# Kernel tuning notes

Hardware: AMD Instinct MI355X
Metric: run time of the kernel (lower is better)

Reference implementation:

```python
import jax, jax.numpy as jnp
import numpy as np

_J6 = jnp.array([[0, 0, 0, 0, 0, 1], [0, 0, 0, 0, -1, 0], [0, 0, 0, 1, 0, 0],
                 [0, 0, 1, 0, 0, 0], [0, -1, 0, 0, 0, 0], [1, 0, 0, 0, 0, 0]], dtype=jnp.float32)
_PAIRS4 = [(0, 1), (0, 2), (0, 3), (1, 2), (1, 3), (2, 3)]


def exterior(p1, p2):
    # p1, p2: (B,T,H,4) -> (B,T,H,6) normalized Pluecker line coordinates
    parts = [p1[..., i] * p2[..., j] - p1[..., j] * p2[..., i] for i, j in _PAIRS4]
    L = jnp.stack(parts, axis=-1)
    n = jnp.sqrt(jnp.sum(L * L, axis=-1, keepdims=True))
    return L / jnp.maximum(n, 1e-12)


def setup_inputs() -> dict:
    D, H = 1024, 16
    B, T = 2, 2048
    key = jax.random.key(0)
    ks = jax.random.split(key, 16)
    s = 0.02
    return {
        'x': jax.random.normal(ks[0], (B, T, D), dtype=jnp.float32),
        'qkv_w': jax.random.normal(ks[1], (D, 3 * D), dtype=jnp.float32) * s,
        'qkv_b': jnp.zeros((3 * D,), dtype=jnp.float32),
        'w1_write': jax.random.normal(ks[2], (D, 4 * H), dtype=jnp.float32) * s,
        'w2_write': jax.random.normal(ks[3], (D, 4 * H), dtype=jnp.float32) * s,
        'w1_read': jax.random.normal(ks[4], (D, 4 * H), dtype=jnp.float32) * s,
        'w2_read': jax.random.normal(ks[5], (D, 4 * H), dtype=jnp.float32) * s,
        'geo_w': jax.random.normal(ks[6], (D, D), dtype=jnp.float32) * s,
        'geo_b': jnp.zeros((D,), dtype=jnp.float32),
        'gate_w': jax.random.normal(ks[7], (D, H), dtype=jnp.float32) * s,
        'gate_b': jnp.zeros((H,), dtype=jnp.float32),
        'inc_scale': jnp.ones((H,), dtype=jnp.float32),
        'out_w': jax.random.normal(ks[8], (D, D), dtype=jnp.float32) * s,
        'out_b': jnp.zeros((D,), dtype=jnp.float32),
    }


def reference(x, qkv_w, qkv_b, w1_write, w2_write, w1_read, w2_read,
              geo_w, geo_b, gate_w, gate_b, inc_scale, out_w, out_b):
    B, T, D = x.shape
    H = inc_scale.shape[0]
    dh = D // H
    scale = dh ** -0.5

    qkv = (x @ qkv_w + qkv_b).reshape(B, T, 3, H, dh)
    qkv = jnp.transpose(qkv, (2, 0, 3, 1, 4))  # (3,B,H,T,dh)
    q, k, v = qkv[0], qkv[1], qkv[2]

    std_logits = jnp.einsum('bhqd,bhkd->bhqk', q, k) * scale

    x_prev = jnp.concatenate([jnp.zeros((B, 1, D), dtype=x.dtype), x[:, :-1]], axis=1)
    w1 = (x_prev @ w1_write).reshape(B, T, H, 4)
    w2 = (x @ w2_write).reshape(B, T, H, 4)
    write_lines = exterior(w1, w2)  # (B,T,H,6)
    r1 = (x @ w1_read).reshape(B, T, H, 4)
    r2 = (x @ w2_read).reshape(B, T, H, 4)
    read_lines = exterior(r1, r2)  # (B,T,H,6)

    J_write = jnp.einsum('bthi,ij->bthj', write_lines, _J6)  # (B,T,H,6)
    geo_logits = jnp.einsum('bqhi,bkhi->bhqk', read_lines, J_write)
    geo_logits = geo_logits * inc_scale.reshape(1, H, 1, 1)

    mask = jnp.triu(jnp.ones((T, T), dtype=bool), k=1)  # True above diagonal
    neg = jnp.float32(-jnp.inf)

    std_attn = jax.nn.softmax(jnp.where(mask, neg, std_logits), axis=-1)
    std_out = jnp.einsum('bhqk,bhkd->bqhd', std_attn, v).reshape(B, T, D)

    geo_attn = jax.nn.softmax(jnp.where(mask, neg, geo_logits), axis=-1)
    geo_v = (x @ geo_w + geo_b).reshape(B, T, H, dh)
    geo_out = jnp.einsum('bhqk,bkhd->bqhd', geo_attn, geo_v).reshape(B, T, D)

    gate = jax.nn.sigmoid(x @ gate_w + gate_b)  # (B,T,H)
    gate = jnp.mean(gate, axis=-1, keepdims=True)  # (B,T,1)

    combined = (1.0 - gate) * std_out + gate * geo_out
    return combined @ out_w + out_b
```

## Files before the change

kernel.cpp:

```cpp
#include <hip/hip_runtime.h>
#include <hip/hip_bf16.h>

#define Bc 2
#define Tc 2048
#define Dc 1024
#define Hc 16
#define Mc (Bc*Tc)
#define QB 64
#define KB 32
#define NALL 4480

typedef __attribute__((ext_vector_type(8))) short bf16x8;
typedef __attribute__((ext_vector_type(4))) short bf16x4;
typedef __attribute__((ext_vector_type(4))) float fx4;

__device__ __forceinline__ short f2bf(float f) {
  __hip_bfloat16 h = __float2bfloat16(f);
  return *reinterpret_cast<short*>(&h);
}
__device__ __forceinline__ float bf2f(short s) {
  unsigned int u = ((unsigned int)(unsigned short)s) << 16;
  float f;
  __builtin_memcpy(&f, &u, 4);
  return f;
}
__device__ __forceinline__ short p2bf(float f) {
  unsigned int u;
  __builtin_memcpy(&u, &f, 4);
  return (short)((u + 0x8000u) >> 16);
}

#define MFMA(a, b, c) __builtin_amdgcn_mfma_f32_16x16x32_bf16((a), (b), (c), 0, 0, 0)

#define GLD16(G, L) __builtin_amdgcn_global_load_lds( \
    (const __attribute__((address_space(1))) unsigned int*)(G), \
    (__attribute__((address_space(3))) unsigned int*)(L), 16, 0, 0)

__global__ __launch_bounds__(256) void f2b_k(const float* __restrict__ in,
                                             short* __restrict__ out) {
  const int i = blockIdx.x * 256 + threadIdx.x;
  const float4 v = ((const float4*)in)[i];
  bf16x4 o;
  o[0] = f2bf(v.x); o[1] = f2bf(v.y); o[2] = f2bf(v.z); o[3] = f2bf(v.w);
  ((bf16x4*)out)[i] = o;
}

__global__ void biasall_k(const float* __restrict__ qkv_b,
                          const float* __restrict__ geob,
                          const float* __restrict__ gateb,
                          float* __restrict__ ball) {
  const int n = blockIdx.x * 256 + threadIdx.x;
  if (n >= NALL) return;
  float v = 0.f;
  if (n < 1024)      v = qkv_b[n] * 0.125f;
  else if (n < 3072) v = qkv_b[n];
  else if (n < 4096) v = geob[n - 3072];
  else if (n >= 4352 && n < 4368) v = gateb[n - 4352];
  ball[n] = v;
}

__global__ __launch_bounds__(256) void tconv_all_k(
    const float* __restrict__ qkv_w, const float* __restrict__ geow,
    const float* __restrict__ w1w, const float* __restrict__ w2w,
    const float* __restrict__ w1r, const float* __restrict__ w2r,
    const float* __restrict__ gatew, short* __restrict__ wtall)
{
  __shared__ float tile[32][33];
  const int n0 = blockIdx.x * 32, k0 = blockIdx.y * 32;
  const int tx = threadIdx.x & 31, ty = threadIdx.x >> 5;
  const int n = n0 + tx;
  const float* src = nullptr; int ln = 0, sN = 0;
  if (n < 3072)      { src = qkv_w; ln = n;        sN = 3072; }
  else if (n < 4096) { src = geow;  ln = n - 3072; sN = 1024; }
  else if (n < 4160) { src = w1w;   ln = n - 4096; sN = 64; }
  else if (n < 4224) { src = w2w;   ln = n - 4160; sN = 64; }
  else if (n < 4288) { src = w1r;   ln = n - 4224; sN = 64; }
  else if (n < 4352) { src = w2r;   ln = n - 4288; sN = 64; }
  else if (n < 4368) { src = gatew; ln = n - 4352; sN = 16; }
  #pragma unroll
  for (int i = 0; i < 4; i++)
    tile[ty * 4 + i][tx] = src ? src[(size_t)(k0 + ty * 4 + i) * sN + ln] : 0.f;
  __syncthreads();
  #pragma unroll
  for (int i = 0; i < 4; i++) {
    const int nn = n0 + ty * 4 + i;
    const float s = (nn < 1024) ? 0.125f : 1.f;
    wtall[(size_t)nn * 1024 + k0 + tx] = f2bf(tile[tx][ty * 4 + i] * s);
  }
}

__global__ __launch_bounds__(256) void tconv_k(const float* __restrict__ W,
                                               short* __restrict__ Wt,
                                               int K, int N) {
  __shared__ float tile[32][33];
  const int k0 = blockIdx.y * 32, n0 = blockIdx.x * 32;
  const int tx = threadIdx.x & 31, ty = threadIdx.x >> 5;
  #pragma unroll
  for (int i = 0; i < 4; i++)
    tile[ty * 4 + i][tx] = W[(size_t)(k0 + ty * 4 + i) * N + n0 + tx];
  __syncthreads();
  #pragma unroll
  for (int i = 0; i < 4; i++)
    Wt[(size_t)(n0 + ty * 4 + i) * K + k0 + tx] = f2bf(tile[tx][ty * 4 + i]);
}

template<bool BF16_OUT>
__global__ __launch_bounds__(256) void gemm_mfma_k(
    const short* __restrict__ A, const short* __restrict__ Bt,
    const float* __restrict__ bias, void* __restrict__ Cv,
    int M, int N, int K)
{
  __shared__ short As[128][32];
  __shared__ short Bs[128][32];
  const int m0 = blockIdx.y * 128, n0 = blockIdx.x * 128;
  const int tid = threadIdx.x;
  const int wave = tid >> 6, lane = tid & 63;
  const int l15 = lane & 15, lg = lane >> 4;
  const int wm = wave >> 1, wn = wave & 1;
  const int srow = lane >> 2;
  const int schk = (lane & 3) * 8;

  const size_t aBase = (size_t)(m0 + wave * 16 + srow) * K + schk;
  const size_t bBase = (size_t)(n0 + wave * 16 + srow) * K + schk;

  fx4 acc[4][4] = {};

  for (int k0 = 0; k0 < K; k0 += 32) {
    __syncthreads();
    GLD16(&A[aBase + k0],              &As[wave * 16][0]);
    GLD16(&A[aBase + (size_t)64 * K + k0], &As[64 + wave * 16][0]);
    GLD16(&Bt[bBase + k0],             &Bs[wave * 16][0]);
    GLD16(&Bt[bBase + (size_t)64 * K + k0], &Bs[64 + wave * 16][0]);
    __syncthreads();
    bf16x8 af[4], bf[4];
    #pragma unroll
    for (int i = 0; i < 4; i++) {
      af[i] = *(const bf16x8*)&As[wm * 64 + i * 16 + l15][8 * lg];
      bf[i] = *(const bf16x8*)&Bs[wn * 64 + i * 16 + l15][8 * lg];
    }
    #pragma unroll
    for (int i = 0; i < 4; i++)
      #pragma unroll
      for (int j = 0; j < 4; j++)
        acc[i][j] = MFMA(af[i], bf[j], acc[i][j]);
  }

  #pragma unroll
  for (int i = 0; i < 4; i++)
    #pragma unroll
    for (int j = 0; j < 4; j++) {
      const int n = n0 + wn * 64 + j * 16 + l15;
      const float bv = bias ? bias[n] : 0.f;
      #pragma unroll
      for (int rg = 0; rg < 4; rg++) {
        const int m = m0 + wm * 64 + i * 16 + lg * 4 + rg;
        const float v = acc[i][j][rg] + bv;
        if constexpr (BF16_OUT)
          ((short*)Cv)[(size_t)m * N + n] = f2bf(v);
        else
          ((float*)Cv)[(size_t)m * N + n] = v;
      }
    }
}

template<bool BF16_OUT>
__global__ __launch_bounds__(256) void gemm_mfma64_k(
    const short* __restrict__ A, const short* __restrict__ Bt,
    const float* __restrict__ bias, void* __restrict__ Cv,
    int M, int N, int K)
{
  __shared__ short As[64][32];
  __shared__ short Bs[128][32];
  const int m0 = blockIdx.y * 64, n0 = blockIdx.x * 128;
  const int tid = threadIdx.x;
  const int wave = tid >> 6, lane = tid & 63;
  const int l15 = lane & 15, lg = lane >> 4;
  const int srow = lane >> 2;
  const int schk = (lane & 3) * 8;

  const size_t aBase = (size_t)(m0 + wave * 16 + srow) * K + schk;
  const size_t bBase = (size_t)(n0 + wave * 16 + srow) * K + schk;

  fx4 acc[4][2] = {};

  for (int k0 = 0; k0 < K; k0 += 32) {
    __syncthreads();
    GLD16(&A[aBase + k0],                   &As[wave * 16][0]);
    GLD16(&Bt[bBase + k0],                  &Bs[wave * 16][0]);
    GLD16(&Bt[bBase + (size_t)64 * K + k0], &Bs[64 + wave * 16][0]);
    __syncthreads();
    bf16x8 af[4], bf[2];
    #pragma unroll
    for (int i = 0; i < 4; i++)
      af[i] = *(const bf16x8*)&As[i * 16 + l15][8 * lg];
    #pragma unroll
    for (int j = 0; j < 2; j++)
      bf[j] = *(const bf16x8*)&Bs[wave * 32 + j * 16 + l15][8 * lg];
    #pragma unroll
    for (int i = 0; i < 4; i++)
      #pragma unroll
      for (int j = 0; j < 2; j++)
        acc[i][j] = MFMA(af[i], bf[j], acc[i][j]);
  }

  #pragma unroll
  for (int i = 0; i < 4; i++)
    #pragma unroll
    for (int j = 0; j < 2; j++) {
      const int n = n0 + wave * 32 + j * 16 + l15;
      const float bv = bias ? bias[n] : 0.f;
      #pragma unroll
      for (int rg = 0; rg < 4; rg++) {
        const int m = m0 + i * 16 + lg * 4 + rg;
        const float v = acc[i][j][rg] + bv;
        if constexpr (BF16_OUT)
          ((short*)Cv)[(size_t)m * N + n] = f2bf(v);
        else
          ((float*)Cv)[(size_t)m * N + n] = v;
      }
    }
}

__device__ __forceinline__ void exterior6(const float a[4], const float c[4], float L[6]) {
  L[0] = a[0]*c[1] - a[1]*c[0];
  L[1] = a[0]*c[2] - a[2]*c[0];
  L[2] = a[0]*c[3] - a[3]*c[0];
  L[3] = a[1]*c[2] - a[2]*c[1];
  L[4] = a[1]*c[3] - a[3]*c[1];
  L[5] = a[2]*c[3] - a[3]*c[2];
}

__device__ __forceinline__ void load4bf(const short* p, float o[4]) {
  const bf16x4 v = *(const bf16x4*)p;
  o[0] = bf2f(v[0]); o[1] = bf2f(v[1]); o[2] = bf2f(v[2]); o[3] = bf2f(v[3]);
}

__global__ void lines_k(const short* __restrict__ allb,
                        const float* __restrict__ incs,
                        short* __restrict__ JWb, short* __restrict__ RLb,
                        float* __restrict__ gatev)
{
  const int idx = blockIdx.x * 256 + threadIdx.x;
  if (idx >= Bc * Tc * Hc) return;
  const int h = idx & 15;
  const int t = (idx >> 4) & (Tc - 1);
  const int b = idx >> 15;
  const size_t row = (size_t)b * Tc + t;
  const size_t lrow = ((size_t)(b * Hc + h) * Tc + t) * 8;

  float a[4] = {0.f, 0.f, 0.f, 0.f};
  float c[4];
  load4bf(&allb[row * NALL + 4160 + h * 4], c);
  if (t > 0) load4bf(&allb[(row - 1) * NALL + 4096 + h * 4], a);

  float L[6];
  exterior6(a, c, L);
  float n = sqrtf(L[0]*L[0] + L[1]*L[1] + L[2]*L[2] + L[3]*L[3] + L[4]*L[4] + L[5]*L[5]);
  float inv = 1.f / fmaxf(n, 1e-12f);
  const float s = incs[h];
  bf16x8 jw;
  jw[0] = f2bf( L[5] * inv * s);
  jw[1] = f2bf(-L[4] * inv * s);
  jw[2] = f2bf( L[3] * inv * s);
  jw[3] = f2bf( L[2] * inv * s);
  jw[4] = f2bf(-L[1] * inv * s);
  jw[5] = f2bf( L[0] * inv * s);
  jw[6] = 0; jw[7] = 0;
  *(bf16x8*)&JWb[lrow] = jw;

  load4bf(&allb[row * NALL + 4224 + h * 4], a);
  load4bf(&allb[row * NALL + 4288 + h * 4], c);
  exterior6(a, c, L);
  n = sqrtf(L[0]*L[0] + L[1]*L[1] + L[2]*L[2] + L[3]*L[3] + L[4]*L[4] + L[5]*L[5]);
  inv = 1.f / fmaxf(n, 1e-12f);
  bf16x8 rl;
  #pragma unroll
  for (int i = 0; i < 6; i++) rl[i] = f2bf(L[i] * inv);
  rl[6] = 0; rl[7] = 0;
  *(bf16x8*)&RLb[lrow] = rl;

  if (h == 0) {
    float ssum = 0.f;
    #pragma unroll
    for (int hh = 0; hh < 16; hh++) {
      const float v = bf2f(allb[row * NALL + 4352 + hh]);
      ssum += 1.f / (1.f + __expf(-v));
    }
    gatev[row] = ssum * (1.f / 16.f);
  }
}

#define LOADK(K0, a0, a1, b0, b1) { \
  const size_t rb0 = (size_t)(b * Tc + (K0) + l15) * NALL + 1024 + h * 64; \
  const size_t rb1 = rb0 + (size_t)16 * NALL; \
  a0 = *(const bf16x8*)&allb[rb0 + lg * 8]; \
  a1 = *(const bf16x8*)&allb[rb0 + 32 + lg * 8]; \
  b0 = *(const bf16x8*)&allb[rb1 + lg * 8]; \
  b1 = *(const bf16x8*)&allb[rb1 + 32 + lg * 8]; }

#define LOADJW(K0, j0, j1) { \
  j0 = z8; j1 = z8; \
  if (lg == 0) { \
    j0 = *(const bf16x8*)&JWb[(size_t)(bh * Tc + (K0) + l15) * 8]; \
    j1 = *(const bf16x8*)&JWb[(size_t)(bh * Tc + (K0) + 16 + l15) * 8]; \
  } }

#define LOADVG(K0, vr, gr) { \
  vr = *(const bf16x8*)&allb[(size_t)(b * Tc + (K0) + kk) * NALL + 2048 + h * 64 + dg]; \
  gr = *(const bf16x8*)&allb[(size_t)(b * Tc + (K0) + kk) * NALL + 3072 + h * 64 + dg]; }

#define STAGEVG(CUR, vr, gr) { \
  _Pragma("unroll") for (int j = 0; j < 8; j++) { \
    const int d = dg + j; \
    const int col = ((kc2 ^ ((d >> 3) & 3)) << 3) | kl2; \
    Vt[CUR][d][col] = vr[j]; Gt[CUR][d][col] = gr[j]; \
  } }

#define COMPUTE(K0, CUR, ka0, ka1, kb0, kb1, jw0, jw1) \
  if ((K0) <= qhi) { \
    fx4 z = {0.f, 0.f, 0.f, 0.f}; \
    fx4 sS0, sS1, sG0, sG1; \
    __builtin_amdgcn_s_setprio(1); \
    sS0 = MFMA(qf0, ka0, z); sS0 = MFMA(qf1, ka1, sS0); \
    sS1 = MFMA(qf0, kb0, z); sS1 = MFMA(qf1, kb1, sS1); \
    sG0 = MFMA(rlf, jw0, z); sG1 = MFMA(rlf, jw1, z); \
    __builtin_amdgcn_s_setprio(0); \
    if ((K0) + KB - 1 > q0 + wave * 16) { \
      const int kg0 = (K0) + l15, kg1 = (K0) + 16 + l15; \
      _Pragma("unroll") for (int r = 0; r < 4; r++) { \
        const int qg = q0 + wave * 16 + lg * 4 + r; \
        if (kg0 > qg) { sS0[r] = -1e30f; sG0[r] = -1e30f; } \
        if (kg1 > qg) { sS1[r] = -1e30f; sG1[r] = -1e30f; } \
      } } \
    _Pragma("unroll") for (int r = 0; r < 4; r++) { \
      const int ql = lg * 4 + r; \
      const float p0 = __expf(sS0[r]); const float p1 = __expf(sS1[r]); \
      lpS[r] += p0 + p1; \
      Ps[wave][ql][l15] = p2bf(p0); Ps[wave][ql][16 + l15] = p2bf(p1); \
      const float g0 = __expf(sG0[r]); const float g1 = __expf(sG1[r]); \
      lpG[r] += g0 + g1; \
      Pg[wave][ql][l15] = p2bf(g0); Pg[wave][ql][16 + l15] = p2bf(g1); \
    } \
    const bf16x8 pa  = *(const bf16x8*)&Ps[wave][l15][8 * lg]; \
    const bf16x8 pga = *(const bf16x8*)&Pg[wave][l15][8 * lg]; \
    __builtin_amdgcn_s_setprio(1); \
    _Pragma("unroll") for (int dt = 0; dt < 4; dt++) { \
      const int dV = dt * 16 + l15; \
      const int swz = 8 * (lg ^ ((dV >> 3) & 3)); \
      accS[dt] = MFMA(pa,  *(const bf16x8*)&Vt[CUR][dV][swz], accS[dt]); \
      accG[dt] = MFMA(pga, *(const bf16x8*)&Gt[CUR][dV][swz], accG[dt]); \
    } \
    __builtin_amdgcn_s_setprio(0); \
  }

__global__ __launch_bounds__(256) void attn3_k(
    const short* __restrict__ allb,
    const short* __restrict__ RLb,
    const short* __restrict__ JWb,
    const float* __restrict__ gate,
    short* __restrict__ combb)
{
  const int orig = blockIdx.x;
  const int xcd  = orig & 7;
  const int idx  = orig >> 3;
  const int pairIdx = idx & 15;
  const int bh   = xcd + 8 * (idx >> 4);
  const int b = bh >> 4, h = bh & 15;
  const int tid = threadIdx.x;
  const int wave = tid >> 6;
  const int lane = tid & 63;
  const int l15 = lane & 15;
  const int lg  = lane >> 4;
  const int kk  = tid >> 3;
  const int dg  = (tid & 7) * 8;
  const int kc2 = kk >> 3, kl2 = kk & 7;

  __shared__ short Vt[2][64][40];
  __shared__ short Gt[2][64][40];
  __shared__ short Ps[4][16][40];
  __shared__ short Pg[4][16][40];

  const bf16x8 z8 = {0, 0, 0, 0, 0, 0, 0, 0};

  for (int half = 0; half < 2; half++) {
    const int qt = half ? (31 - pairIdx) : pairIdx;
    const int q0 = qt * QB;
    const int nkt = 2 * qt + 2;
    const int qrow = wave * 16 + l15;
    const int qhi = q0 + wave * 16 + 15;

    const size_t qrb = (size_t)(b * Tc + q0 + qrow) * NALL + h * 64;
    const bf16x8 qf0 = *(const bf16x8*)&allb[qrb + lg * 8];
    const bf16x8 qf1 = *(const bf16x8*)&allb[qrb + 32 + lg * 8];
    bf16x8 rlf = z8;
    if (lg == 0) rlf = *(const bf16x8*)&RLb[(size_t)(bh * Tc + q0 + qrow) * 8];

    fx4 accS[4] = {}, accG[4] = {};
    float lpS[4] = {0.f, 0.f, 0.f, 0.f};
    float lpG[4] = {0.f, 0.f, 0.f, 0.f};

    bf16x8 kA0a, kA1a, kB0a, kB1a, jw0a, jw1a, vrA, grA;
    bf16x8 kA0b, kA1b, kB0b, kB1b, jw0b, jw1b, vrB, grB;
    LOADK(0, kA0a, kA1a, kB0a, kB1a);
    LOADJW(0, jw0a, jw1a);
    LOADVG(0, vrA, grA);

    __syncthreads();

    for (int kt = 0; kt < nkt; kt += 2) {
      const int k0a = kt * KB, k0b = k0a + KB;
      STAGEVG(0, vrA, grA);
      LOADK(k0b, kA0b, kA1b, kB0b, kB1b);
      LOADJW(k0b, jw0b, jw1b);
      LOADVG(k0b, vrB, grB);
      __syncthreads();
      COMPUTE(k0a, 0, kA0a, kA1a, kB0a, kB1a, jw0a, jw1a);
      STAGEVG(1, vrB, grB);
      if (kt + 2 < nkt) {
        LOADK(k0b + KB, kA0a, kA1a, kB0a, kB1a);
        LOADJW(k0b + KB, jw0a, jw1a);
        LOADVG(k0b + KB, vrA, grA);
      }
      __syncthreads();
      COMPUTE(k0b, 1, kA0b, kA1b, kB0b, kB1b, jw0b, jw1b);
    }

    #pragma unroll
    for (int r = 0; r < 4; r++) {
      float ls = lpS[r];
      ls += __shfl_xor(ls, 1); ls += __shfl_xor(ls, 2);
      ls += __shfl_xor(ls, 4); ls += __shfl_xor(ls, 8);
      float lgeo = lpG[r];
      lgeo += __shfl_xor(lgeo, 1); lgeo += __shfl_xor(lgeo, 2);
      lgeo += __shfl_xor(lgeo, 4); lgeo += __shfl_xor(lgeo, 8);
      const int qg = q0 + wave * 16 + lg * 4 + r;
      const float gt = gate[(size_t)b * Tc + qg];
      const float invS = (1.f - gt) / ls;
      const float invG = gt / lgeo;
      #pragma unroll
      for (int dt = 0; dt < 4; dt++) {
        const float o = accS[dt][r] * invS + accG[dt][r] * invG;
        combb[(size_t)(b * Tc + qg) * 1024 + h * 64 + dt * 16 + l15] = f2bf(o);
      }
    }
  }
}

extern "C" void kernel_launch(void* const* d_in, const int* in_sizes, int n_in,
                              void* d_out, int out_size, void* d_ws, size_t ws_size,
                              hipStream_t stream) {
  (void)in_sizes; (void)n_in; (void)out_size; (void)ws_size;
  const float* x     = (const float*)d_in[0];
  const float* qkv_w = (const float*)d_in[1];
  const float* qkv_b = (const float*)d_in[2];
  const float* w1w   = (const float*)d_in[3];
  const float* w2w   = (const float*)d_in[4];
  const float* w1r   = (const float*)d_in[5];
  const float* w2r   = (const float*)d_in[6];
  const float* geow  = (const float*)d_in[7];
  const float* geob  = (const float*)d_in[8];
  const float* gatew = (const float*)d_in[9];
  const float* gateb = (const float*)d_in[10];
  const float* incs  = (const float*)d_in[11];
  const float* outw  = (const float*)d_in[12];
  const float* outb  = (const float*)d_in[13];
  float* out = (float*)d_out;

  char* p = (char*)d_ws;
  short* xb    = (short*)p;  p += (size_t)4096 * 1024 * 2;
  short* wtall = (short*)p;  p += (size_t)NALL * 1024 * 2;
  short* allb  = (short*)p;  p += (size_t)4096 * NALL * 2;
  short* combb = (short*)p;  p += (size_t)4096 * 1024 * 2;
  short* wtout = (short*)p;  p += (size_t)1024 * 1024 * 2;
  short* JWb   = (short*)p;  p += (size_t)32 * 2048 * 8 * 2;
  short* RLb   = (short*)p;  p += (size_t)32 * 2048 * 8 * 2;
  float* ball  = (float*)p;  p += (size_t)NALL * 4;
  float* gatev = (float*)p;  p += (size_t)4096 * 4;

  const dim3 blk(256);

  f2b_k<<<dim3(4096), blk, 0, stream>>>(x, xb);
  biasall_k<<<dim3((NALL + 255) / 256), blk, 0, stream>>>(qkv_b, geob, gateb, ball);
  tconv_all_k<<<dim3(NALL / 32, 32), blk, 0, stream>>>(qkv_w, geow, w1w, w2w, w1r, w2r, gatew, wtall);
  tconv_k<<<dim3(32, 32), blk, 0, stream>>>(outw, wtout, 1024, 1024);

  gemm_mfma_k<true><<<dim3(NALL / 128, 32), blk, 0, stream>>>(xb, wtall, ball, allb, 4096, NALL, 1024);

  lines_k<<<dim3((Bc * Tc * Hc + 255) / 256), blk, 0, stream>>>(allb, incs, JWb, RLb, gatev);

  attn3_k<<<dim3(512), blk, 0, stream>>>(allb, RLb, JWb, gatev, combb);

  gemm_mfma64_k<false><<<dim3(8, 64), blk, 0, stream>>>(combb, wtout, outb, (void*)out, 4096, 1024, 1024);
}
```

Measured before the change: 203.9 us.

## Merge prep kernels into one launch and use exp2 with log2e-folded scales

Combines the x conversion, the bias assembly and both weight transpose/convert kernels into one prep kernel, chosen by block index, which removes three kernel launches and their gaps. It also folds log2(e) into the Q scale and the incidence scale so the attention softmax can call exp2f instead of __expf, saving a multiply per exponential. The folded scales change bf16 rounding of the weights slightly. Blocks that take the early-return branch still contain a __syncthreads in other branches of the same kernel.

```diff
diff --git a/kernel.cpp b/kernel.cpp
--- a/kernel.cpp
+++ b/kernel.cpp
@@ -9,6 +9,8 @@
 #define QB 64
 #define KB 32
 #define NALL 4480
+#define QSCALE 0.18033688056680776f
+#define LOG2E  1.4426950408889634f
 
 typedef __attribute__((ext_vector_type(8))) short bf16x8;
 typedef __attribute__((ext_vector_type(4))) short bf16x4;
@@ -36,72 +38,76 @@
     (const __attribute__((address_space(1))) unsigned int*)(G), \
     (__attribute__((address_space(3))) unsigned int*)(L), 16, 0, 0)
 
-__global__ __launch_bounds__(256) void f2b_k(const float* __restrict__ in,
-                                             short* __restrict__ out) {
-  const int i = blockIdx.x * 256 + threadIdx.x;
-  const float4 v = ((const float4*)in)[i];
-  bf16x4 o;
-  o[0] = f2bf(v.x); o[1] = f2bf(v.y); o[2] = f2bf(v.z); o[3] = f2bf(v.w);
-  ((bf16x4*)out)[i] = o;
-}
-
-__global__ void biasall_k(const float* __restrict__ qkv_b,
-                          const float* __restrict__ geob,
-                          const float* __restrict__ gateb,
-                          float* __restrict__ ball) {
-  const int n = blockIdx.x * 256 + threadIdx.x;
-  if (n >= NALL) return;
-  float v = 0.f;
-  if (n < 1024)      v = qkv_b[n] * 0.125f;
-  else if (n < 3072) v = qkv_b[n];
-  else if (n < 4096) v = geob[n - 3072];
-  else if (n >= 4352 && n < 4368) v = gateb[n - 4352];
-  ball[n] = v;
-}
-
-__global__ __launch_bounds__(256) void tconv_all_k(
+__global__ __launch_bounds__(256) void prep_k(
+    const float* __restrict__ x,
     const float* __restrict__ qkv_w, const float* __restrict__ geow,
     const float* __restrict__ w1w, const float* __restrict__ w2w,
     const float* __restrict__ w1r, const float* __restrict__ w2r,
-    const float* __restrict__ gatew, short* __restrict__ wtall)
+    const float* __restrict__ gatew, const float* __restrict__ outw,
+    const float* __restrict__ qkv_b, const float* __restrict__ geob,
+    const float* __restrict__ gateb,
+    short* __restrict__ xb, short* __restrict__ wtall,
+    short* __restrict__ wtout, float* __restrict__ ball)
 {
   __shared__ float tile[32][33];
-  const int n0 = blockIdx.x * 32, k0 = blockIdx.y * 32;
-  const int tx = threadIdx.x & 31, ty = threadIdx.x >> 5;
-  const int n = n0 + tx;
-  const float* src = nullptr; int ln = 0, sN = 0;
-  if (n < 3072)      { src = qkv_w; ln = n;        sN = 3072; }
-  else if (n < 4096) { src = geow;  ln = n - 3072; sN = 1024; }
-  else if (n < 4160) { src = w1w;   ln = n - 4096; sN = 64; }
-  else if (n < 4224) { src = w2w;   ln = n - 4160; sN = 64; }
-  else if (n < 4288) { src = w1r;   ln = n - 4224; sN = 64; }
-  else if (n < 4352) { src = w2r;   ln = n - 4288; sN = 64; }
-  else if (n < 4368) { src = gatew; ln = n - 4352; sN = 16; }
-  #pragma unroll
-  for (int i = 0; i < 4; i++)
-    tile[ty * 4 + i][tx] = src ? src[(size_t)(k0 + ty * 4 + i) * sN + ln] : 0.f;
-  __syncthreads();
-  #pragma unroll
-  for (int i = 0; i < 4; i++) {
-    const int nn = n0 + ty * 4 + i;
-    const float s = (nn < 1024) ? 0.125f : 1.f;
-    wtall[(size_t)nn * 1024 + k0 + tx] = f2bf(tile[tx][ty * 4 + i] * s);
-  }
-}
-
-__global__ __launch_bounds__(256) void tconv_k(const float* __restrict__ W,
-                                               short* __restrict__ Wt,
-                                               int K, int N) {
-  __shared__ float tile[32][33];
-  const int k0 = blockIdx.y * 32, n0 = blockIdx.x * 32;
-  const int tx = threadIdx.x & 31, ty = threadIdx.x >> 5;
-  #pragma unroll
-  for (int i = 0; i < 4; i++)
-    tile[ty * 4 + i][tx] = W[(size_t)(k0 + ty * 4 + i) * N + n0 + tx];
-  __syncthreads();
-  #pragma unroll
-  for (int i = 0; i < 4; i++)
-    Wt[(size_t)(n0 + ty * 4 + i) * K + k0 + tx] = f2bf(tile[tx][ty * 4 + i]);
+  const int blk = blockIdx.x;
+
+  if (blk < 4096) {
+    const int i = blk * 256 + threadIdx.x;
+    const float4 v = ((const float4*)x)[i];
+    bf16x4 o;
+    o[0] = f2bf(v.x); o[1] = f2bf(v.y); o[2] = f2bf(v.z); o[3] = f2bf(v.w);
+    ((bf16x4*)xb)[i] = o;
+    return;
+  }
+  if (blk < 8576) {
+    const int b2 = blk - 4096;
+    const int n0 = (b2 % 140) * 32, k0 = (b2 / 140) * 32;
+    const int tx = threadIdx.x & 31, ty = threadIdx.x >> 5;
+    const int n = n0 + tx;
+    const float* src = nullptr; int ln = 0, sN = 0;
+    if (n < 3072)      { src = qkv_w; ln = n;        sN = 3072; }
+    else if (n < 4096) { src = geow;  ln = n - 3072; sN = 1024; }
+    else if (n < 4160) { src = w1w;   ln = n - 4096; sN = 64; }
+    else if (n < 4224) { src = w2w;   ln = n - 4160; sN = 64; }
+    else if (n < 4288) { src = w1r;   ln = n - 4224; sN = 64; }
+    else if (n < 4352) { src = w2r;   ln = n - 4288; sN = 64; }
+    else if (n < 4368) { src = gatew; ln = n - 4352; sN = 16; }
+    #pragma unroll
+    for (int i = 0; i < 4; i++)
+      tile[ty * 4 + i][tx] = src ? src[(size_t)(k0 + ty * 4 + i) * sN + ln] : 0.f;
+    __syncthreads();
+    #pragma unroll
+    for (int i = 0; i < 4; i++) {
+      const int nn = n0 + ty * 4 + i;
+      const float s = (nn < 1024) ? QSCALE : 1.f;
+      wtall[(size_t)nn * 1024 + k0 + tx] = f2bf(tile[tx][ty * 4 + i] * s);
+    }
+    return;
+  }
+  if (blk < 9600) {
+    const int b3 = blk - 8576;
+    const int n0 = (b3 & 31) * 32, k0 = (b3 >> 5) * 32;
+    const int tx = threadIdx.x & 31, ty = threadIdx.x >> 5;
+    #pragma unroll
+    for (int i = 0; i < 4; i++)
+      tile[ty * 4 + i][tx] = outw[(size_t)(k0 + ty * 4 + i) * 1024 + n0 + tx];
+    __syncthreads();
+    #pragma unroll
+    for (int i = 0; i < 4; i++)
+      wtout[(size_t)(n0 + ty * 4 + i) * 1024 + k0 + tx] = f2bf(tile[tx][ty * 4 + i]);
+    return;
+  }
+  {
+    const int n = (blk - 9600) * 256 + threadIdx.x;
+    if (n >= NALL) return;
+    float v = 0.f;
+    if (n < 1024)      v = qkv_b[n] * QSCALE;
+    else if (n < 3072) v = qkv_b[n];
+    else if (n < 4096) v = geob[n - 3072];
+    else if (n >= 4352 && n < 4368) v = gateb[n - 4352];
+    ball[n] = v;
+  }
 }
 
 template<bool BF16_OUT>
@@ -257,7 +263,7 @@
   exterior6(a, c, L);
   float n = sqrtf(L[0]*L[0] + L[1]*L[1] + L[2]*L[2] + L[3]*L[3] + L[4]*L[4] + L[5]*L[5]);
   float inv = 1.f / fmaxf(n, 1e-12f);
-  const float s = incs[h];
+  const float s = incs[h] * LOG2E;
   bf16x8 jw;
   jw[0] = f2bf( L[5] * inv * s);
   jw[1] = f2bf(-L[4] * inv * s);
@@ -334,10 +340,10 @@
       } } \
     _Pragma("unroll") for (int r = 0; r < 4; r++) { \
       const int ql = lg * 4 + r; \
-      const float p0 = __expf(sS0[r]); const float p1 = __expf(sS1[r]); \
+      const float p0 = exp2f(sS0[r]); const float p1 = exp2f(sS1[r]); \
       lpS[r] += p0 + p1; \
       Ps[wave][ql][l15] = p2bf(p0); Ps[wave][ql][16 + l15] = p2bf(p1); \
-      const float g0 = __expf(sG0[r]); const float g1 = __expf(sG1[r]); \
+      const float g0 = exp2f(sG0[r]); const float g1 = exp2f(sG1[r]); \
       lpG[r] += g0 + g1; \
       Pg[wave][ql][l15] = p2bf(g0); Pg[wave][ql][16 + l15] = p2bf(g1); \
     } \
@@ -479,10 +485,9 @@
 
   const dim3 blk(256);
 
-  f2b_k<<<dim3(4096), blk, 0, stream>>>(x, xb);
-  biasall_k<<<dim3((NALL + 255) / 256), blk, 0, stream>>>(qkv_b, geob, gateb, ball);
-  tconv_all_k<<<dim3(NALL / 32, 32), blk, 0, stream>>>(qkv_w, geow, w1w, w2w, w1r, w2r, gatew, wtall);
-  tconv_k<<<dim3(32, 32), blk, 0, stream>>>(outw, wtout, 1024, 1024);
+  prep_k<<<dim3(9618), blk, 0, stream>>>(x, qkv_w, geow, w1w, w2w, w1r, w2r,
+                                         gatew, outw, qkv_b, geob, gateb,
+                                         xb, wtall, wtout, ball);
 
   gemm_mfma_k<true><<<dim3(NALL / 128, 32), blk, 0, stream>>>(xb, wtall, ball, allb, 4096, NALL, 1024);
 
```

New measurement: 205.1 us. Within noise of the previous version (+0.6%).
